# Kernel tuning notes

Measured on AMD Instinct MI355X. Metric: run time of the kernel, lower is better.

The kernel has to match this reference:

```python
import jax, jax.numpy as jnp
import numpy as np

N_HEADS = 16
NOPE = 128
ROPE = 64
VDIM = 128
HEAD_DIM = NOPE + ROPE  # 192


def apply_rope(x, cos, sin):
    # x: [B, S, H, D] with D even; pairs (a, b) rotated by complex freqs.
    B, S, H, D = x.shape
    xr = x.reshape(B, S, H, D // 2, 2)
    a, b = xr[..., 0], xr[..., 1]
    c = cos[None, :, None, :]
    s = sin[None, :, None, :]
    out = jnp.stack([a * c - b * s, a * s + b * c], axis=-1)
    return out.reshape(B, S, H, D)


def setup_inputs() -> dict:
    key = jax.random.key(0)
    ks = jax.random.split(key, 8)
    B, S, DIM = 1, 2048, 2048
    x = jax.random.normal(ks[0], (B, S, DIM), dtype=jnp.float32)
    wq = jax.random.normal(ks[1], (N_HEADS * HEAD_DIM, DIM), dtype=jnp.float32) * (DIM ** -0.5)
    wk = jax.random.normal(ks[2], (N_HEADS * HEAD_DIM, DIM), dtype=jnp.float32) * (DIM ** -0.5)
    wv = jax.random.normal(ks[3], (N_HEADS * VDIM, DIM), dtype=jnp.float32) * (DIM ** -0.5)
    wo = jax.random.normal(ks[4], (DIM, N_HEADS * VDIM), dtype=jnp.float32) * ((N_HEADS * VDIM) ** -0.5)
    # rotary freqs: theta = 10000^{-2i/d}, angles = pos * theta
    inv_freq = 1.0 / (10000.0 ** (np.arange(0, ROPE, 2, dtype=np.float32) / ROPE))
    angles = np.arange(S, dtype=np.float32)[:, None] * inv_freq[None, :]  # [S, 32]
    freqs_cos = jnp.asarray(np.cos(angles))
    freqs_sin = jnp.asarray(np.sin(angles))
    # additive causal mask
    mask = jnp.where(jnp.triu(jnp.ones((S, S), dtype=bool), k=1), -1e9, 0.0).astype(jnp.float32)
    return {"x": x, "wq": wq, "wk": wk, "wv": wv, "wo": wo,
            "freqs_cos": freqs_cos, "freqs_sin": freqs_sin, "mask": mask, "start_pos": 0}


def reference(x, wq, wk, wv, wo, freqs_cos, freqs_sin, mask, start_pos):
    B, S, DIM = x.shape
    q = (x @ wq.T).reshape(B, S, N_HEADS, HEAD_DIM)
    k = (x @ wk.T).reshape(B, S, N_HEADS, HEAD_DIM)
    v = (x @ wv.T).reshape(B, S, N_HEADS, VDIM)
    q_nope, q_pe = q[..., :NOPE], q[..., NOPE:]
    k_nope, k_pe = k[..., :NOPE], k[..., NOPE:]
    q_pe = apply_rope(q_pe, freqs_cos, freqs_sin)
    k_pe = apply_rope(k_pe, freqs_cos, freqs_sin)
    scores = (jnp.einsum('bshd,bthd->bsht', q_nope, k_nope)
              + jnp.einsum('bshd,bthd->bsht', q_pe, k_pe)) * (HEAD_DIM ** -0.5)
    scores = scores + mask[None, :, None, :]
    probs = jax.nn.softmax(scores.astype(jnp.float32), axis=-1).astype(x.dtype)
    out = jnp.einsum('bsht,bthd->bshd', probs, v)
    return out.reshape(B, S, N_HEADS * VDIM) @ wo.T
```

## Files before the change

kernel.cpp:

```cpp
#include <hip/hip_runtime.h>
#include <hip/hip_bf16.h>
#include <math.h>

#define NH 16
#define NOPE 128
#define ROPE 64
#define VDIM 128
#define HD 192
#define SEQ 2048
#define DIM 2048
#define QKD (NH * HD)
#define VD  (NH * VDIM)
#define QKVS 8192

typedef __attribute__((ext_vector_type(8))) short short8;
typedef __attribute__((ext_vector_type(4))) short short4v;
typedef __attribute__((ext_vector_type(4))) float f32x4;
typedef unsigned int u32;

#define WAIT_VM8  0x0F78
#define WAIT_VM6  0x0F76
#define WAIT_VM0  0x0F70
#define WAIT_LGKM 0xC07F

static __device__ inline short f2bf(float f) {
  union { float f; unsigned u; } v; v.f = f;
  unsigned r = (v.u + 0x7fffu + ((v.u >> 16) & 1u)) >> 16;
  return (short)r;
}
static __device__ inline float bf2f(unsigned short u) {
  union { unsigned u; float f; } v; v.u = ((unsigned)u) << 16;
  return v.f;
}

static __device__ __forceinline__ void gload16(const short* g, short* l) {
  __builtin_amdgcn_global_load_lds(
      (const __attribute__((address_space(1))) u32*)g,
      (__attribute__((address_space(3))) u32*)l, 16, 0, 0);
}


#define RDA(pp, hh, mh) do { \
  const char* Lb_ = Lsm + ((pp) * 32768) + ((hh) * 16384) + aoff; \
  afr[0] = *(const short8*)(Lb_ + ((mh) * 4096) + 0); \
  afr[1] = *(const short8*)(Lb_ + ((mh) * 4096) + 1024); \
  afr[2] = *(const short8*)(Lb_ + ((mh) * 4096) + 2048); \
  afr[3] = *(const short8*)(Lb_ + ((mh) * 4096) + 3072); \
} while (0)

#define RDB(pp, hh) do { \
  const char* Lb_ = Lsm + 65536 + ((pp) * 32768) + ((hh) * 16384) + boff; \
  bfr[0] = *(const short8*)(Lb_ + 0); \
  bfr[1] = *(const short8*)(Lb_ + 1024); \
  bfr[2] = *(const short8*)(Lb_ + 2048); \
  bfr[3] = *(const short8*)(Lb_ + 3072); \
} while (0)

#define SA(kt, h) do { \
  char* d_ = Lsm + (((kt) & 1) * 32768) + ((h) * 16384) + wv * 1024; \
  gload16(gA0 + (kt) * 64 + (h) * 32, (short*)d_); \
  gload16(gA1 + (kt) * 64 + (h) * 32, (short*)(d_ + 8192)); \
} while (0)

#define SB(kt, h) do { \
  char* d_ = Lsm + 65536 + (((kt) & 1) * 32768) + ((h) * 16384) + wv * 1024; \
  gload16(gB0 + (kt) * 64 + (h) * 32, (short*)d_); \
  gload16(gB1 + (kt) * 64 + (h) * 32, (short*)(d_ + 8192)); \
} while (0)

#define MFMA1(mi, ni) \
  acc[mi][ni] = __builtin_amdgcn_mfma_f32_16x16x32_bf16(afr[(mi) & 3], bfr[ni], acc[mi][ni], 0, 0, 0)

#define MM(mh) do { \
  MFMA1((mh)*4+0, 0); MFMA1((mh)*4+1, 0); MFMA1((mh)*4+2, 0); MFMA1((mh)*4+3, 0); \
  MFMA1((mh)*4+0, 1); MFMA1((mh)*4+1, 1); MFMA1((mh)*4+2, 1); MFMA1((mh)*4+3, 1); \
  MFMA1((mh)*4+0, 2); MFMA1((mh)*4+1, 2); MFMA1((mh)*4+2, 2); MFMA1((mh)*4+3, 2); \
  MFMA1((mh)*4+0, 3); MFMA1((mh)*4+1, 3); MFMA1((mh)*4+2, 3); MFMA1((mh)*4+3, 3); \
} while (0)

#define GBAR() __builtin_amdgcn_s_barrier()
#define GLGKM0() __builtin_amdgcn_s_waitcnt(WAIT_LGKM)
#define GPRIO1() __builtin_amdgcn_s_setprio(1)
#define GPRIO0() __builtin_amdgcn_s_setprio(0)
#define GNOP ((void)0)

#define TILE(pp, S1, S2, S3, S4, VMW) do { \
  RDA(pp, 0, 0); RDB(pp, 0); S1; \
  GBAR(); GLGKM0(); GPRIO1(); MM(0); GPRIO0(); GBAR(); \
  RDA(pp, 0, 1); S2; \
  GBAR(); GLGKM0(); GPRIO1(); MM(1); GPRIO0(); GBAR(); \
  RDA(pp, 1, 0); RDB(pp, 1); S3; \
  GBAR(); GLGKM0(); GPRIO1(); MM(0); GPRIO0(); GBAR(); \
  RDA(pp, 1, 1); S4; \
  GBAR(); GLGKM0(); GPRIO1(); MM(1); GPRIO0(); VMW; GBAR(); \
} while (0)

__global__ __launch_bounds__(512, 2) void gemm256_bt(
    const short* __restrict__ A, const short* __restrict__ B,
    short* __restrict__ C, int K, int lda, int ldb, int ldc) {
  __shared__ __align__(16) char Lsm[131072];

  const int tid = threadIdx.x;
  const int lane = tid & 63;
  const int l15 = lane & 15;
  const int quad = lane >> 4;
  const int wv = tid >> 6;
  const int wr = wv >> 2, wc = wv & 3;

  const int bid = blockIdx.x;
  const int swz = (bid & 7) * 32 + (bid >> 3);
  const int m0 = (swz >> 5) * 256;
  const int n0 = (swz & 31) * 256;

  const short* gA0 = A + (size_t)(m0 + wv * 16 + l15) * lda + quad * 8;
  const short* gA1 = gA0 + (size_t)128 * lda;
  const short* gB0 = B + (size_t)(n0 + wv * 16 + l15) * ldb + quad * 8;
  const short* gB1 = gB0 + (size_t)128 * ldb;

  const int aoff = wr * 8192 + lane * 16;
  const int boff = wc * 4096 + lane * 16;

  f32x4 acc[8][4];
#pragma unroll
  for (int i = 0; i < 8; ++i)
#pragma unroll
    for (int j = 0; j < 4; ++j) acc[i][j] = (f32x4)(0.f);
  short8 afr[4], bfr[4];

  const int NT = K >> 6;

  SB(0, 0); SA(0, 0); SB(0, 1); SA(0, 1);
  SB(1, 0); SA(1, 0); SB(1, 1);
  __builtin_amdgcn_s_waitcnt(WAIT_VM6);
  GBAR();

  int kt = 0;
  for (; kt + 4 <= NT; kt += 2) {
    TILE(0, SA(kt + 1, 1), SB(kt + 2, 0), SA(kt + 2, 0), SB(kt + 2, 1),
         __builtin_amdgcn_s_waitcnt(WAIT_VM6));
    TILE(1, SA(kt + 2, 1), SB(kt + 3, 0), SA(kt + 3, 0), SB(kt + 3, 1),
         __builtin_amdgcn_s_waitcnt(WAIT_VM6));
  }
  TILE(0, SA(kt + 1, 1), GNOP, GNOP, GNOP, __builtin_amdgcn_s_waitcnt(WAIT_VM0));
  TILE(1, GNOP, GNOP, GNOP, GNOP, GNOP);

#pragma unroll
  for (int m = 0; m < 8; ++m) {
    const size_t rb = (size_t)(m0 + wr * 128 + m * 16 + quad * 4) * ldc +
                      n0 + wc * 64 + l15;
#pragma unroll
    for (int n = 0; n < 4; ++n)
#pragma unroll
      for (int r = 0; r < 4; ++r)
        C[rb + (size_t)r * ldc + n * 16] = f2bf(acc[m][n][r]);
  }
}

template <bool BF16OUT>
__global__ __launch_bounds__(256) void gemm_bt(
    const short* __restrict__ A, const short* __restrict__ B,
    void* __restrict__ Cv, int K, int lda, int ldb, int ldc, float oscale) {
  __shared__ __align__(16) short Ls[4][2][4096];

  const int tid = threadIdx.x;
  const int lane = tid & 63;
  const int wave = tid >> 6;
  const int wr = wave >> 1, wc = wave & 1;
  const int lane15 = lane & 15, quad = lane >> 4;
  const int m0 = blockIdx.y * 128, n0 = blockIdx.x * 128;

  const short* gA[4]; const short* gB[4];
#pragma unroll
  for (int i = 0; i < 4; ++i) {
    int gidx = i * 64 + lane;
    int r = gidx >> 2, p = gidx & 3;
    int g = (p ^ ((r >> 1) & 3)) * 8;
    gA[i] = A + (size_t)(m0 + wr * 64 + r) * lda + g;
    gB[i] = B + (size_t)(n0 + wc * 64 + r) * ldb + g;
  }

  f32x4 acc[4][4];
#pragma unroll
  for (int i = 0; i < 4; ++i)
#pragma unroll
    for (int j = 0; j < 4; ++j) acc[i][j] = (f32x4)(0.f);

#pragma unroll
  for (int i = 0; i < 4; ++i) gload16(gA[i], &Ls[wave][0][i * 512]);
#pragma unroll
  for (int i = 0; i < 4; ++i) gload16(gB[i], &Ls[wave][0][2048 + i * 512]);

  const int rsw = (lane15 >> 1) & 3;
  for (int k0 = 0; k0 < K; k0 += 32) {
    const int cur = (k0 >> 5) & 1;
    __builtin_amdgcn_s_waitcnt(WAIT_LGKM);
    if (k0 + 32 < K) {
      const int nxt = cur ^ 1;
#pragma unroll
      for (int i = 0; i < 4; ++i) gload16(gA[i] + k0 + 32, &Ls[wave][nxt][i * 512]);
#pragma unroll
      for (int i = 0; i < 4; ++i) gload16(gB[i] + k0 + 32, &Ls[wave][nxt][2048 + i * 512]);
      __builtin_amdgcn_s_waitcnt(WAIT_VM8);
    } else {
      __builtin_amdgcn_s_waitcnt(WAIT_VM0);
    }
    const short* bufp = &Ls[wave][cur][0];
    short8 af[4], bfv[4];
#pragma unroll
    for (int i = 0; i < 4; ++i)
      af[i] = *(const short8*)&bufp[(i * 16 + lane15) * 32 + (quad ^ rsw) * 8];
#pragma unroll
    for (int j = 0; j < 4; ++j)
      bfv[j] = *(const short8*)&bufp[2048 + (j * 16 + lane15) * 32 + (quad ^ rsw) * 8];
#pragma unroll
    for (int i = 0; i < 4; ++i)
#pragma unroll
      for (int j = 0; j < 4; ++j)
        acc[i][j] = __builtin_amdgcn_mfma_f32_16x16x32_bf16(af[i], bfv[j], acc[i][j], 0, 0, 0);
  }

#pragma unroll
  for (int i = 0; i < 4; ++i)
#pragma unroll
    for (int j = 0; j < 4; ++j)
#pragma unroll
      for (int r = 0; r < 4; ++r) {
        size_t idx = (size_t)(m0 + wr * 64 + i * 16 + quad * 4 + r) * ldc +
                     n0 + wc * 64 + j * 16 + lane15;
        if (BF16OUT)
          ((short*)Cv)[idx] = f2bf(acc[i][j][r] * oscale);
        else
          ((float*)Cv)[idx] = acc[i][j][r];
      }
}

__global__ __launch_bounds__(256) void rope_qk(
    short* __restrict__ qk, const float* __restrict__ cosf, const float* __restrict__ sinf) {
  int idx = blockIdx.x * blockDim.x + threadIdx.x;
  int j = idx & 31;
  int h = (idx >> 5) & (NH - 1);
  int s = idx >> 9;
  if (s >= SEQ) return;

  float c = cosf[s * 32 + j];
  float sn = sinf[s * 32 + j];
  size_t rowb = (size_t)s * QKVS + h * HD + NOPE + 2 * j;

  u32* pq = (u32*)(qk + rowb);
  u32 w = *pq;
  float a = bf2f((unsigned short)(w & 0xffff));
  float b = bf2f((unsigned short)(w >> 16));
  *pq = (u32)(unsigned short)f2bf(a * c - b * sn) |
        ((u32)(unsigned short)f2bf(a * sn + b * c) << 16);

  u32* pk = (u32*)(qk + rowb + QKD);
  w = *pk;
  a = bf2f((unsigned short)(w & 0xffff));
  b = bf2f((unsigned short)(w >> 16));
  *pk = (u32)(unsigned short)f2bf(a * c - b * sn) |
        ((u32)(unsigned short)f2bf(a * sn + b * c) << 16);
}

__global__ __launch_bounds__(256) void bf16_convert(
    const float* __restrict__ in, short* __restrict__ out, int n4) {
  int i = blockIdx.x * 256 + threadIdx.x;
  if (i >= n4) return;
  float4 f = ((const float4*)in)[i];
  short4v o;
  o.x = f2bf(f.x); o.y = f2bf(f.y); o.z = f2bf(f.z); o.w = f2bf(f.w);
  ((short4v*)out)[i] = o;
}

__global__ __launch_bounds__(256) void conv_wqkv(
    const float* __restrict__ wq, const float* __restrict__ wk,
    const float* __restrict__ wv, short* __restrict__ wqkv, int n4) {
  int i = blockIdx.x * 256 + threadIdx.x;
  if (i >= n4) return;
  int row = i >> 9;
  float4 f;
  if (row < QKD) f = ((const float4*)wq)[i];
  else if (row < 2 * QKD) f = ((const float4*)wk)[i - QKD * (DIM / 4)];
  else f = ((const float4*)wv)[i - 2 * QKD * (DIM / 4)];
  short4v o;
  o.x = f2bf(f.x); o.y = f2bf(f.y); o.z = f2bf(f.z); o.w = f2bf(f.w);
  ((short4v*)wqkv)[i] = o;
}

__global__ __launch_bounds__(256) void vt_bf16(
    const short* __restrict__ vb, short* __restrict__ vtb) {
  __shared__ short tile[64][74];
  const int t0 = blockIdx.x * 64;
  const int c0 = blockIdx.y * 64;
  const int tid = threadIdx.x;
#pragma unroll
  for (int i = 0; i < 16; ++i) {
    int idx = i * 256 + tid;
    int r = idx >> 6, c = idx & 63;
    tile[r][c] = vb[(size_t)(t0 + r) * QKVS + c0 + c];
  }
  __syncthreads();
  const int h = c0 >> 7;
  const int dbase = c0 & 127;
#pragma unroll
  for (int i = 0; i < 16; ++i) {
    int idx = i * 256 + tid;
    int d = idx >> 6, t = idx & 63;
    vtb[(size_t)h * VDIM * SEQ + (size_t)(dbase + d) * SEQ + t0 + t] = tile[t][d];
  }
}

#define BQ 64
#define BT 64
#define CHT 8
#define PSTR 76
#define MFIX 8.0f

__global__ __launch_bounds__(256) void attn_part(
    const short* __restrict__ qk,
    const short* __restrict__ vtb,
    short* __restrict__ Opart,
    float* __restrict__ lpart)
{
  __shared__ __align__(16) short Ks[BT * 192];
  __shared__ __align__(16) short Vt[VDIM * 64];
  __shared__ __align__(16) short Ps[4 * 16 * PSTR];

  const int qt = blockIdx.x;
  const int h = blockIdx.y;
  const int chk = blockIdx.z;
  if (chk * CHT > qt) return;

  const int tid = threadIdx.x;
  const int wave = tid >> 6;
  const int lane = tid & 63;
  const int lane15 = lane & 15;
  const int quad = lane >> 4;
  const int bb = qt >> 3;
  const int slot = h * 80 + qt + 4 * bb * (bb - 1) + (qt - 8 * bb) * bb + chk;
  const int R0 = qt * BQ;
  const int kt_beg = chk * CHT;
  const int kt_end = min(kt_beg + CHT, qt + 1);
  const float scale = 0.072168784f;

  const int qrow = R0 + wave * 16 + lane15;
  short8 qf[6];
  const short* qbase = qk + (size_t)qrow * QKVS + h * HD + quad * 8;
#pragma unroll
  for (int kc = 0; kc < 6; ++kc) qf[kc] = *(const short8*)(qbase + kc * 32);

  const short* kb = qk + QKD;
  const short* gK[6]; short* lK[6];
#pragma unroll
  for (int i = 0; i < 6; ++i) {
    int id = i * 256 + tid;
    int row = id / 24, cX = id - row * 24;
    int ch = cX ^ (row & 7);
    lK[i] = &Ks[id * 8];
    gK[i] = kb + (size_t)row * QKVS + h * HD + ch * 8;
  }
  const short* gV[4]; short* lV[4];
#pragma unroll
  for (int i = 0; i < 4; ++i) {
    int id = i * 256 + tid;
    int row = id >> 3, cX = id & 7;
    int ch = cX ^ (row & 7);
    lV[i] = &Vt[id * 8];
    gV[i] = vtb + (size_t)h * VDIM * SEQ + (size_t)row * SEQ + ch * 8;
  }

  f32x4 oacc[8];
#pragma unroll
  for (int i = 0; i < 8; ++i) oacc[i] = (f32x4)(0.f);
  float lsum[4] = {0.f, 0.f, 0.f, 0.f};

  short* pw = &Ps[wave * 16 * PSTR];

  for (int kt = kt_beg; kt < kt_end; ++kt) {
    const int t0 = kt * BT;
    __syncthreads();
#pragma unroll
    for (int i = 0; i < 6; ++i) gload16(gK[i] + (size_t)t0 * QKVS, lK[i]);
#pragma unroll
    for (int i = 0; i < 4; ++i) gload16(gV[i] + t0, lV[i]);
    __syncthreads();

    f32x4 sacc[4];
#pragma unroll
    for (int c = 0; c < 4; ++c) {
      sacc[c] = (f32x4)(0.f);
      const int row = c * 16 + lane15;
#pragma unroll
      for (int kc = 0; kc < 6; ++kc) {
        int cX = (4 * kc + quad) ^ (lane15 & 7);
        short8 kf = *(const short8*)&Ks[row * 192 + cX * 8];
        sacc[c] = __builtin_amdgcn_mfma_f32_16x16x32_bf16(qf[kc], kf, sacc[c], 0, 0, 0);
      }
    }

    if (kt == qt) {
#pragma unroll
      for (int c = 0; c < 4; ++c)
#pragma unroll
        for (int r = 0; r < 4; ++r) {
          int tloc = c * 16 + lane15;
          int qloc = wave * 16 + quad * 4 + r;
          if (tloc > qloc) sacc[c][r] = -1e30f;
        }
    }

#pragma unroll
    for (int c = 0; c < 4; ++c)
#pragma unroll
      for (int r = 0; r < 4; ++r) {
        float p = __expf(sacc[c][r] * scale - MFIX);
        lsum[r] += p;
        pw[(quad * 4 + r) * PSTR + c * 16 + lane15] = f2bf(p);
      }

    short8 pf0 = *(const short8*)&pw[lane15 * PSTR + quad * 8];
    short8 pf1 = *(const short8*)&pw[lane15 * PSTR + 32 + quad * 8];
#pragma unroll
    for (int ch = 0; ch < 8; ++ch) {
      const int row = ch * 16 + lane15;
      int cX0 = quad ^ (lane15 & 7);
      int cX1 = (4 + quad) ^ (lane15 & 7);
      short8 vf0 = *(const short8*)&Vt[row * 64 + cX0 * 8];
      short8 vf1 = *(const short8*)&Vt[row * 64 + cX1 * 8];
      oacc[ch] = __builtin_amdgcn_mfma_f32_16x16x32_bf16(pf0, vf0, oacc[ch], 0, 0, 0);
      oacc[ch] = __builtin_amdgcn_mfma_f32_16x16x32_bf16(pf1, vf1, oacc[ch], 0, 0, 0);
    }
  }

  short* op = Opart + (size_t)slot * (64 * 128);
#pragma unroll
  for (int ch = 0; ch < 8; ++ch)
#pragma unroll
    for (int r = 0; r < 4; ++r)
      op[(wave * 16 + quad * 4 + r) * 128 + ch * 16 + lane15] = f2bf(oacc[ch][r]);

  float red[4];
#pragma unroll
  for (int r = 0; r < 4; ++r) {
    float s = lsum[r];
    s += __shfl_xor(s, 1, 64);
    s += __shfl_xor(s, 2, 64);
    s += __shfl_xor(s, 4, 64);
    s += __shfl_xor(s, 8, 64);
    red[r] = s;
  }
  if (lane15 == 0) {
#pragma unroll
    for (int r = 0; r < 4; ++r)
      lpart[(size_t)slot * 64 + wave * 16 + quad * 4 + r] = red[r];
  }
}

__global__ __launch_bounds__(256) void attn_combine(
    const short* __restrict__ Opart, const float* __restrict__ lpart,
    short* __restrict__ aob) {
  const int qt = blockIdx.x, h = blockIdx.y;
  const int nact = (qt >> 3) + 1;
  const int bb = qt >> 3;
  const int base = h * 80 + qt + 4 * bb * (bb - 1) + (qt - 8 * bb) * bb;
  const int tid = threadIdx.x;
  const int row = tid >> 2;
  const int cg = (tid & 3) * 32;

  float acc[32];
#pragma unroll
  for (int e = 0; e < 32; ++e) acc[e] = 0.f;
  float lsum = 0.f;

  for (int c = 0; c < nact; ++c) {
    const short* sp = Opart + (size_t)(base + c) * (64 * 128) + row * 128 + cg;
    lsum += lpart[(size_t)(base + c) * 64 + row];
#pragma unroll
    for (int g = 0; g < 4; ++g) {
      short8 vv = *(const short8*)(sp + g * 8);
#pragma unroll
      for (int e = 0; e < 8; ++e) acc[g * 8 + e] += bf2f((unsigned short)vv[e]);
    }
  }

  float inv = 1.f / lsum;
#pragma unroll
  for (int g = 0; g < 4; ++g) {
    short8 ov;
#pragma unroll
    for (int e = 0; e < 8; ++e) ov[e] = f2bf(acc[g * 8 + e] * inv);
    *(short8*)(aob + (size_t)(qt * 64 + row) * QKVS + h * 128 + cg + g * 8) = ov;
  }
}

extern "C" void kernel_launch(void* const* d_in, const int* in_sizes, int n_in,
                              void* d_out, int out_size, void* d_ws, size_t ws_size,
                              hipStream_t stream) {
  const float* x  = (const float*)d_in[0];
  const float* wq = (const float*)d_in[1];
  const float* wk = (const float*)d_in[2];
  const float* wv = (const float*)d_in[3];
  const float* wo = (const float*)d_in[4];
  const float* fc = (const float*)d_in[5];
  const float* fs = (const float*)d_in[6];

  char* ws8 = (char*)d_ws;
  short* xb    = (short*)(ws8 + 0);
  short* wo_b  = (short*)(ws8 + 0);
  short* wqkv  = (short*)(ws8 + 8388608);
  short* vtb   = (short*)(ws8 + 8388608);
  short* Opart = (short*)(ws8 + 16777216);
  float* lpart = (float*)(ws8 + 37748736);
  short* qkv   = (short*)(ws8 + 41943040);
  float* out   = (float*)d_out;

  const int NX4 = DIM * DIM / 4;
  const int NQKV4 = QKVS * DIM / 4;
  const int ROPE_GRID = (SEQ * NH * 32) / 256;

  bf16_convert<<<(NX4 + 255) / 256, 256, 0, stream>>>(x, xb, NX4);
  conv_wqkv<<<(NQKV4 + 255) / 256, 256, 0, stream>>>(wq, wk, wv, wqkv, NQKV4);

  gemm256_bt<<<dim3((QKVS / 256) * (SEQ / 256)), 512, 0, stream>>>(
      xb, wqkv, qkv, DIM, DIM, DIM, QKVS);
  rope_qk<<<ROPE_GRID, 256, 0, stream>>>(qkv, fc, fs);
  vt_bf16<<<dim3(SEQ / 64, VD / 64), 256, 0, stream>>>(qkv + 2 * QKD, vtb);

  bf16_convert<<<(NX4 + 255) / 256, 256, 0, stream>>>(wo, wo_b, NX4);

  attn_part<<<dim3(SEQ / BQ, NH, 4), 256, 0, stream>>>(qkv, vtb, Opart, lpart);
  attn_combine<<<dim3(SEQ / BQ, NH), 256, 0, stream>>>(Opart, lpart, qkv + 2 * QKD);

  gemm_bt<false><<<dim3(DIM / 128, SEQ / 128), 256, 0, stream>>>(
      qkv + 2 * QKD, wo_b, out, DIM, QKVS, DIM, DIM, 1.0f);
}
```

Before: 348.1 us.

## Double-buffer K tiles and remap attention blocks in attn_part

```diff
diff --git a/kernel.cpp b/kernel.cpp
--- a/kernel.cpp
+++ b/kernel.cpp
@@ -20,6 +20,7 @@
 
 #define WAIT_VM8  0x0F78
 #define WAIT_VM6  0x0F76
+#define WAIT_VM4  0x0F74
 #define WAIT_VM0  0x0F70
 #define WAIT_LGKM 0xC07F
 
@@ -321,13 +322,15 @@
     short* __restrict__ Opart,
     float* __restrict__ lpart)
 {
-  __shared__ __align__(16) short Ks[BT * 192];
+  __shared__ __align__(16) short Ks[2][BT * 192];
   __shared__ __align__(16) short Vt[VDIM * 64];
   __shared__ __align__(16) short Ps[4 * 16 * PSTR];
 
-  const int qt = blockIdx.x;
-  const int h = blockIdx.y;
-  const int chk = blockIdx.z;
+  const int bid = blockIdx.x;
+  const int i0 = bid >> 3;
+  const int h = (bid & 7) + ((i0 >> 7) << 3);
+  const int qt = (i0 & 127) >> 2;
+  const int chk = i0 & 3;
   if (chk * CHT > qt) return;
 
   const int tid = threadIdx.x;
@@ -347,15 +350,16 @@
   const short* qbase = qk + (size_t)qrow * QKVS + h * HD + quad * 8;
 #pragma unroll
   for (int kc = 0; kc < 6; ++kc) qf[kc] = *(const short8*)(qbase + kc * 32);
+  __builtin_amdgcn_sched_barrier(0);
 
   const short* kb = qk + QKD;
-  const short* gK[6]; short* lK[6];
+  int lKoff[6]; const short* gK[6];
 #pragma unroll
   for (int i = 0; i < 6; ++i) {
     int id = i * 256 + tid;
     int row = id / 24, cX = id - row * 24;
     int ch = cX ^ (row & 7);
-    lK[i] = &Ks[id * 8];
+    lKoff[i] = id * 8;
     gK[i] = kb + (size_t)row * QKVS + h * HD + ch * 8;
   }
   const short* gV[4]; short* lV[4];
@@ -375,16 +379,30 @@
 
   short* pw = &Ps[wave * 16 * PSTR];
 
+  {
+    const size_t t0 = (size_t)kt_beg * BT;
+#pragma unroll
+    for (int i = 0; i < 6; ++i) gload16(gK[i] + t0 * QKVS, &Ks[0][lKoff[i]]);
+#pragma unroll
+    for (int i = 0; i < 4; ++i) gload16(gV[i] + t0, lV[i]);
+  }
+  __builtin_amdgcn_s_waitcnt(WAIT_VM0);
+  __builtin_amdgcn_s_barrier();
+  __builtin_amdgcn_sched_barrier(0);
+
   for (int kt = kt_beg; kt < kt_end; ++kt) {
-    const int t0 = kt * BT;
-    __syncthreads();
-#pragma unroll
-    for (int i = 0; i < 6; ++i) gload16(gK[i] + (size_t)t0 * QKVS, lK[i]);
-#pragma unroll
-    for (int i = 0; i < 4; ++i) gload16(gV[i] + t0, lV[i]);
-    __syncthreads();
-
+    const int cur = (kt - kt_beg) & 1;
+    const bool have = (kt + 1 < kt_end);
+
+    if (have) {
+      const size_t tn = (size_t)(kt + 1) * BT;
+#pragma unroll
+      for (int i = 0; i < 6; ++i) gload16(gK[i] + tn * QKVS, &Ks[cur ^ 1][lKoff[i]]);
+    }
+
+    const short* kcur = &Ks[cur][0];
     f32x4 sacc[4];
+    __builtin_amdgcn_s_setprio(1);
 #pragma unroll
     for (int c = 0; c < 4; ++c) {
       sacc[c] = (f32x4)(0.f);
@@ -392,10 +410,11 @@
 #pragma unroll
       for (int kc = 0; kc < 6; ++kc) {
         int cX = (4 * kc + quad) ^ (lane15 & 7);
-        short8 kf = *(const short8*)&Ks[row * 192 + cX * 8];
+        short8 kf = *(const short8*)&kcur[row * 192 + cX * 8];
         sacc[c] = __builtin_amdgcn_mfma_f32_16x16x32_bf16(qf[kc], kf, sacc[c], 0, 0, 0);
       }
     }
+    __builtin_amdgcn_s_setprio(0);
 
     if (kt == qt) {
 #pragma unroll
@@ -419,6 +438,13 @@
 
     short8 pf0 = *(const short8*)&pw[lane15 * PSTR + quad * 8];
     short8 pf1 = *(const short8*)&pw[lane15 * PSTR + 32 + quad * 8];
+
+    if (have) __builtin_amdgcn_s_waitcnt(WAIT_VM6);
+    else      __builtin_amdgcn_s_waitcnt(WAIT_VM0);
+    __builtin_amdgcn_s_barrier();
+    __builtin_amdgcn_sched_barrier(0);
+
+    __builtin_amdgcn_s_setprio(1);
 #pragma unroll
     for (int ch = 0; ch < 8; ++ch) {
       const int row = ch * 16 + lane15;
@@ -428,6 +454,18 @@
       short8 vf1 = *(const short8*)&Vt[row * 64 + cX1 * 8];
       oacc[ch] = __builtin_amdgcn_mfma_f32_16x16x32_bf16(pf0, vf0, oacc[ch], 0, 0, 0);
       oacc[ch] = __builtin_amdgcn_mfma_f32_16x16x32_bf16(pf1, vf1, oacc[ch], 0, 0, 0);
+    }
+    __builtin_amdgcn_s_setprio(0);
+
+    if (have) {
+      __builtin_amdgcn_s_waitcnt(WAIT_LGKM);
+      __builtin_amdgcn_s_barrier();
+      const size_t tn = (size_t)(kt + 1) * BT;
+#pragma unroll
+      for (int i = 0; i < 4; ++i) gload16(gV[i] + tn, lV[i]);
+      __builtin_amdgcn_s_waitcnt(WAIT_VM4);
+      __builtin_amdgcn_s_barrier();
+      __builtin_amdgcn_sched_barrier(0);
     }
   }
 
@@ -527,7 +565,7 @@
 
   bf16_convert<<<(NX4 + 255) / 256, 256, 0, stream>>>(wo, wo_b, NX4);
 
-  attn_part<<<dim3(SEQ / BQ, NH, 4), 256, 0, stream>>>(qkv, vtb, Opart, lpart);
+  attn_part<<<dim3(2048), 256, 0, stream>>>(qkv, vtb, Opart, lpart);
   attn_combine<<<dim3(SEQ / BQ, NH), 256, 0, stream>>>(Opart, lpart, qkv + 2 * QKD);
 
   gemm_bt<false><<<dim3(DIM / 128, SEQ / 128), 256, 0, stream>>>(
```

Result: no change. 351.0 us (+0.8%).

## Use 128-row query tiles with 512-thread blocks and compact XCD-aware attention grid

Applied to the files above, without the earlier changes.

```diff
diff --git a/kernel.cpp b/kernel.cpp
--- a/kernel.cpp
+++ b/kernel.cpp
@@ -309,37 +309,41 @@
   }
 }
 
-#define BQ 64
+#define BQ 128
 #define BT 64
 #define CHT 8
 #define PSTR 76
 #define MFIX 8.0f
 
-__global__ __launch_bounds__(256) void attn_part(
+__global__ __launch_bounds__(512, 4) void attn_part(
     const short* __restrict__ qk,
     const short* __restrict__ vtb,
     short* __restrict__ Opart,
     float* __restrict__ lpart)
 {
   __shared__ __align__(16) short Ks[BT * 192];
-  __shared__ __align__(16) short Vt[VDIM * 64];
-  __shared__ __align__(16) short Ps[4 * 16 * PSTR];
-
-  const int qt = blockIdx.x;
-  const int h = blockIdx.y;
-  const int chk = blockIdx.z;
-  if (chk * CHT > qt) return;
+  __shared__ __align__(16) short Vt[VDIM * BT];
+  __shared__ __align__(16) short Ps[8 * 16 * PSTR];
+
+  const int xcd = blockIdx.x;
+  const int i0 = blockIdx.y;
+  const int h = xcd + ((i0 >= 40) ? 8 : 0);
+  int jj = (i0 >= 40) ? (i0 - 40) : i0;
+  int qtb = 15;
+  while (jj >= (qtb >> 2) + 1) { jj -= (qtb >> 2) + 1; --qtb; }
+  const int chk = jj;
 
   const int tid = threadIdx.x;
   const int wave = tid >> 6;
   const int lane = tid & 63;
   const int lane15 = lane & 15;
   const int quad = lane >> 4;
-  const int bb = qt >> 3;
-  const int slot = h * 80 + qt + 4 * bb * (bb - 1) + (qt - 8 * bb) * bb + chk;
-  const int R0 = qt * BQ;
+  const int g = qtb >> 2;
+  const int slot = h * 40 + (g + 1) * (2 * g + (qtb & 3)) + chk;
+  const int R0 = qtb * BQ;
+  const int NT = 2 * qtb + 2;
   const int kt_beg = chk * CHT;
-  const int kt_end = min(kt_beg + CHT, qt + 1);
+  const int kt_end = min(kt_beg + CHT, NT);
   const float scale = 0.072168784f;
 
   const int qrow = R0 + wave * 16 + lane15;
@@ -349,19 +353,19 @@
   for (int kc = 0; kc < 6; ++kc) qf[kc] = *(const short8*)(qbase + kc * 32);
 
   const short* kb = qk + QKD;
-  const short* gK[6]; short* lK[6];
-#pragma unroll
-  for (int i = 0; i < 6; ++i) {
-    int id = i * 256 + tid;
+  int lKoff[3]; const short* gK[3];
+#pragma unroll
+  for (int i = 0; i < 3; ++i) {
+    int id = i * 512 + tid;
     int row = id / 24, cX = id - row * 24;
     int ch = cX ^ (row & 7);
-    lK[i] = &Ks[id * 8];
+    lKoff[i] = id * 8;
     gK[i] = kb + (size_t)row * QKVS + h * HD + ch * 8;
   }
-  const short* gV[4]; short* lV[4];
-#pragma unroll
-  for (int i = 0; i < 4; ++i) {
-    int id = i * 256 + tid;
+  const short* gV[2]; short* lV[2];
+#pragma unroll
+  for (int i = 0; i < 2; ++i) {
+    int id = i * 512 + tid;
     int row = id >> 3, cX = id & 7;
     int ch = cX ^ (row & 7);
     lV[i] = &Vt[id * 8];
@@ -379,12 +383,13 @@
     const int t0 = kt * BT;
     __syncthreads();
 #pragma unroll
-    for (int i = 0; i < 6; ++i) gload16(gK[i] + (size_t)t0 * QKVS, lK[i]);
-#pragma unroll
-    for (int i = 0; i < 4; ++i) gload16(gV[i] + t0, lV[i]);
+    for (int i = 0; i < 3; ++i) gload16(gK[i] + (size_t)t0 * QKVS, &Ks[lKoff[i]]);
+#pragma unroll
+    for (int i = 0; i < 2; ++i) gload16(gV[i] + t0, lV[i]);
     __syncthreads();
 
     f32x4 sacc[4];
+    __builtin_amdgcn_s_setprio(1);
 #pragma unroll
     for (int c = 0; c < 4; ++c) {
       sacc[c] = (f32x4)(0.f);
@@ -396,15 +401,16 @@
         sacc[c] = __builtin_amdgcn_mfma_f32_16x16x32_bf16(qf[kc], kf, sacc[c], 0, 0, 0);
       }
     }
-
-    if (kt == qt) {
+    __builtin_amdgcn_s_setprio(0);
+
+    if (kt >= 2 * qtb) {
 #pragma unroll
       for (int c = 0; c < 4; ++c)
 #pragma unroll
         for (int r = 0; r < 4; ++r) {
-          int tloc = c * 16 + lane15;
-          int qloc = wave * 16 + quad * 4 + r;
-          if (tloc > qloc) sacc[c][r] = -1e30f;
+          int tg = t0 + c * 16 + lane15;
+          int qg = R0 + wave * 16 + quad * 4 + r;
+          if (tg > qg) sacc[c][r] = -1e30f;
         }
     }
 
@@ -419,6 +425,7 @@
 
     short8 pf0 = *(const short8*)&pw[lane15 * PSTR + quad * 8];
     short8 pf1 = *(const short8*)&pw[lane15 * PSTR + 32 + quad * 8];
+    __builtin_amdgcn_s_setprio(1);
 #pragma unroll
     for (int ch = 0; ch < 8; ++ch) {
       const int row = ch * 16 + lane15;
@@ -429,9 +436,10 @@
       oacc[ch] = __builtin_amdgcn_mfma_f32_16x16x32_bf16(pf0, vf0, oacc[ch], 0, 0, 0);
       oacc[ch] = __builtin_amdgcn_mfma_f32_16x16x32_bf16(pf1, vf1, oacc[ch], 0, 0, 0);
     }
-  }
-
-  short* op = Opart + (size_t)slot * (64 * 128);
+    __builtin_amdgcn_s_setprio(0);
+  }
+
+  short* op = Opart + (size_t)slot * (128 * 128);
 #pragma unroll
   for (int ch = 0; ch < 8; ++ch)
 #pragma unroll
@@ -451,17 +459,19 @@
   if (lane15 == 0) {
 #pragma unroll
     for (int r = 0; r < 4; ++r)
-      lpart[(size_t)slot * 64 + wave * 16 + quad * 4 + r] = red[r];
+      lpart[(size_t)slot * 128 + wave * 16 + quad * 4 + r] = red[r];
   }
 }
 
 __global__ __launch_bounds__(256) void attn_combine(
     const short* __restrict__ Opart, const float* __restrict__ lpart,
     short* __restrict__ aob) {
-  const int qt = blockIdx.x, h = blockIdx.y;
-  const int nact = (qt >> 3) + 1;
-  const int bb = qt >> 3;
-  const int base = h * 80 + qt + 4 * bb * (bb - 1) + (qt - 8 * bb) * bb;
+  const int qt64 = blockIdx.x, h = blockIdx.y;
+  const int qtb = qt64 >> 1;
+  const int half = qt64 & 1;
+  const int g = qtb >> 2;
+  const int nact = g + 1;
+  const int base = h * 40 + (g + 1) * (2 * g + (qtb & 3));
   const int tid = threadIdx.x;
   const int row = tid >> 2;
   const int cg = (tid & 3) * 32;
@@ -472,23 +482,24 @@
   float lsum = 0.f;
 
   for (int c = 0; c < nact; ++c) {
-    const short* sp = Opart + (size_t)(base + c) * (64 * 128) + row * 128 + cg;
-    lsum += lpart[(size_t)(base + c) * 64 + row];
-#pragma unroll
-    for (int g = 0; g < 4; ++g) {
-      short8 vv = *(const short8*)(sp + g * 8);
-#pragma unroll
-      for (int e = 0; e < 8; ++e) acc[g * 8 + e] += bf2f((unsigned short)vv[e]);
+    const short* sp = Opart + (size_t)(base + c) * (128 * 128) +
+                      (half * 64 + row) * 128 + cg;
+    lsum += lpart[(size_t)(base + c) * 128 + half * 64 + row];
+#pragma unroll
+    for (int gg = 0; gg < 4; ++gg) {
+      short8 vv = *(const short8*)(sp + gg * 8);
+#pragma unroll
+      for (int e = 0; e < 8; ++e) acc[gg * 8 + e] += bf2f((unsigned short)vv[e]);
     }
   }
 
   float inv = 1.f / lsum;
 #pragma unroll
-  for (int g = 0; g < 4; ++g) {
+  for (int gg = 0; gg < 4; ++gg) {
     short8 ov;
 #pragma unroll
-    for (int e = 0; e < 8; ++e) ov[e] = f2bf(acc[g * 8 + e] * inv);
-    *(short8*)(aob + (size_t)(qt * 64 + row) * QKVS + h * 128 + cg + g * 8) = ov;
+    for (int e = 0; e < 8; ++e) ov[e] = f2bf(acc[gg * 8 + e] * inv);
+    *(short8*)(aob + (size_t)(qt64 * 64 + row) * QKVS + h * 128 + cg + gg * 8) = ov;
   }
 }
 
@@ -527,8 +538,8 @@
 
   bf16_convert<<<(NX4 + 255) / 256, 256, 0, stream>>>(wo, wo_b, NX4);
 
-  attn_part<<<dim3(SEQ / BQ, NH, 4), 256, 0, stream>>>(qkv, vtb, Opart, lpart);
-  attn_combine<<<dim3(SEQ / BQ, NH), 256, 0, stream>>>(Opart, lpart, qkv + 2 * QKD);
+  attn_part<<<dim3(8, 80), 512, 0, stream>>>(qkv, vtb, Opart, lpart);
+  attn_combine<<<dim3(SEQ / 64, NH), 256, 0, stream>>>(Opart, lpart, qkv + 2 * QKD);
 
   gemm_bt<false><<<dim3(DIM / 128, SEQ / 128), 256, 0, stream>>>(
       qkv + 2 * QKD, wo_b, out, DIM, QKVS, DIM, DIM, 1.0f);
```

After: 329.6 us. 1.06x faster.
